# Kernel optimization log

Hardware: AMD Instinct MI355X
Metric: run time of the kernel (lower is better)

Reference implementation:

```python
import jax, jax.numpy as jnp
import numpy as np

B, N = 64, 128          # batch, nodes
D = 3                   # feature_dim
E = 1                   # edge_dim
M = 16                  # m_dim (lucidrains EGNN default)
L = 2                   # number_of_layers
EIN = 2 * D + 1 + E     # edge MLP input dim = 8


def setup_inputs() -> dict:
    key = jax.random.key(0)
    ks = jax.random.split(key, 24)
    s = 0.1

    def w(k, shape):
        return jax.random.normal(k, shape, dtype=jnp.float32) * s

    return {
        "t": jax.random.uniform(ks[0], (B, N, 1), dtype=jnp.float32),
        "coors": jax.random.normal(ks[1], (B, N, 2), dtype=jnp.float32),
        "vel": jax.random.normal(ks[2], (B, N, 2), dtype=jnp.float32),
        # per-layer EGNN params, stacked over L layers
        "We1": w(ks[3], (L, EIN, 2 * EIN)), "be1": jnp.zeros((L, 2 * EIN), jnp.float32),
        "We2": w(ks[4], (L, 2 * EIN, M)),   "be2": jnp.zeros((L, M), jnp.float32),
        "Wc1": w(ks[5], (L, M, 4 * M)),     "bc1": jnp.zeros((L, 4 * M), jnp.float32),
        "Wc2": w(ks[6], (L, 4 * M, 1)),     "bc2": jnp.zeros((L, 1), jnp.float32),
        "Wv": w(ks[7], (L, D, 1)),          "bv": jnp.ones((L, 1), jnp.float32),
        # 1x1 conv head (kernel size 1 -> plain channel matmul)
        "Wconv1": w(ks[8], (32, 4)), "bconv1": jnp.zeros((32,), jnp.float32),
        "Wconv2": w(ks[9], (4, 32)), "bconv2": jnp.zeros((4,), jnp.float32),
    }


def _egnn_forward(t, coors, vel, We1, be1, We2, be2, Wc1, bc1, Wc2, bc2, Wv, bv,
                  Wconv1, bconv1, Wconv2, bconv2):
    silu = jax.nn.silu
    selu = jax.nn.selu
    b, n, _ = coors.shape
    feats = jnp.broadcast_to(t, (b, n, D))          # t.repeat(1,1,feature_dim)
    edges = jnp.ones((b, n, n, E), dtype=coors.dtype)
    hi = jnp.broadcast_to(feats[:, :, None, :], (b, n, n, D))
    hj = jnp.broadcast_to(feats[:, None, :, :], (b, n, n, D))

    for l in range(L):
        rel = coors[:, :, None, :] - coors[:, None, :, :]      # b i j 2
        dist = jnp.sum(rel * rel, axis=-1, keepdims=True)      # b i j 1
        e_in = jnp.concatenate([hi, hj, dist, edges], axis=-1) # b i j 8
        # edge MLP: Linear -> SiLU -> Linear -> SiLU
        m = silu(e_in @ We1[l] + be1[l])
        m = silu(m @ We2[l] + be2[l])                          # b i j M
        # coors MLP: SiLU -> Linear -> SiLU -> Linear -> scalar weight per edge
        h = silu(silu(m) @ Wc1[l] + bc1[l])
        w_ij = (h @ Wc2[l] + bc2[l])[..., 0]                   # b i j
        agg = jnp.einsum('bij,bijc->bic', w_ij, rel)           # b i 2
        # velocity update: phi_v(h_i) * v_i + aggregated relative-coor messages
        phi_v = feats @ Wv[l] + bv[l]                          # b n 1
        vel = phi_v * vel + agg
        coors = coors + vel
        # EGNN_layer wrapper applies SELU to coors and vel
        coors = selu(coors)
        vel = selu(vel)

    # conv head: concat channels (coors 2 + vel 2 = 4), two 1x1 convs
    x = selu(jnp.concatenate([coors, vel], axis=-1))           # b n 4
    x = selu(jnp.einsum('bnc,oc->bno', x, Wconv1) + bconv1)    # b n 32
    y = jnp.einsum('bnc,oc->bno', x, Wconv2) + bconv2          # b n 4
    return y[..., 0:2], y[..., 2:4]


def reference(t, coors, vel, We1, be1, We2, be2, Wc1, bc1, Wc2, bc2, Wv, bv,
              Wconv1, bconv1, Wconv2, bconv2):
    return _egnn_forward(t, coors, vel, We1, be1, We2, be2, Wc1, bc1, Wc2, bc2,
                         Wv, bv, Wconv1, bconv1, Wconv2, bconv2)
```

## Files before the change

kernel.cpp:

```cpp
#include <hip/hip_runtime.h>


#define NB 64
#define NN 128

typedef __attribute__((ext_vector_type(8))) short short8;
typedef __attribute__((ext_vector_type(4))) float floatx4;

__device__ __forceinline__ unsigned short f2bf(float x) {
    unsigned u = __float_as_uint(x);
    return (unsigned short)((u + 0x7FFFu + ((u >> 16) & 1u)) >> 16);
}
__device__ __forceinline__ float bf2f(unsigned short b) {
    return __uint_as_float(((unsigned)b) << 16);
}
__device__ __forceinline__ unsigned pack2(float x, float y) {
    return (unsigned)f2bf(x) | ((unsigned)f2bf(y) << 16);
}
__device__ __forceinline__ float silu_f(float x) {
    float e = __expf(-x);
    return x * __builtin_amdgcn_rcpf(1.0f + e);
}
__device__ __forceinline__ float selu_f(float x) {
    const float alpha = 1.6732632423543772f;
    const float scale = 1.0507009873554805f;
    float neg = alpha * (__expf(x) - 1.0f);
    return scale * (x > 0.0f ? x : neg);
}

template <bool DO_HEAD>
__global__ __launch_bounds__(256) void egnn_layer(
    const float* __restrict__ t,
    const float* __restrict__ coors_in,
    const float* __restrict__ vel_in,
    const float* __restrict__ We1, const float* __restrict__ be1,
    const float* __restrict__ We2, const float* __restrict__ be2,
    const float* __restrict__ Wc1, const float* __restrict__ bc1,
    const float* __restrict__ Wc2, const float* __restrict__ bc2,
    const float* __restrict__ Wv,  const float* __restrict__ bv,
    const float* __restrict__ Wconv1, const float* __restrict__ bconv1,
    const float* __restrict__ Wconv2, const float* __restrict__ bconv2,
    int layer,
    float* __restrict__ coors_out, float* __restrict__ vel_out,
    float* __restrict__ out)
{
    const int l   = threadIdx.x & 63;
    const int wv  = threadIdx.x >> 6;
    const int row = blockIdx.x * 4 + wv;
    const int b   = row >> 7;
    const int i   = row & 127;
    const int q   = l >> 4;
    const int em  = l & 15;

    const float* We1l = We1 + layer * 8 * 16;
    const float* be1l = be1 + layer * 16;
    const float* We2l = We2 + layer * 16 * 16;
    const float* be2l = be2 + layer * 16;
    const float* Wc1l = Wc1 + layer * 16 * 64;
    const float* bc1l = bc1 + layer * 64;
    const float* Wc2l = Wc2 + layer * 64;
    const float  wv_s = Wv[layer * 3 + 0] + Wv[layer * 3 + 1] + Wv[layer * 3 + 2];
    const float  bvl  = bv[layer];

    float Aw = We1l[0 * 16 + em] + We1l[1 * 16 + em] + We1l[2 * 16 + em];
    float Bw = We1l[3 * 16 + em] + We1l[4 * 16 + em] + We1l[5 * 16 + em];
    float Cw = We1l[6 * 16 + em];
    unsigned short Ah = f2bf(Aw), Al = f2bf(Aw - bf2f(Ah));
    unsigned short Bh = f2bf(Bw), Bl = f2bf(Bw - bf2f(Bh));
    unsigned short Ch = f2bf(Cw), Cl = f2bf(Cw - bf2f(Ch));
    short8 wA;
    {
        short h0 = (q == 0) ? (short)Ah : ((q == 1) ? (short)Al : (short)0);
        short h1 = (q == 0) ? (short)Bh : ((q == 1) ? (short)Bl : (short)0);
        short h2 = (q == 0) ? (short)Ch : ((q == 1) ? (short)Cl : (short)0);
        wA[0] = h0; wA[1] = h0; wA[2] = h1; wA[3] = h1;
        wA[4] = h2; wA[5] = h2; wA[6] = 0;  wA[7] = 0;
    }
    floatx4 biasA;
#pragma unroll
    for (int r = 0; r < 4; ++r)
        biasA[r] = We1l[7 * 16 + 4 * q + r] + be1l[4 * q + r];

    short8 wB;
#pragma unroll
    for (int j = 0; j < 8; ++j) {
        int k = q * 8 + j;
        float w = We2l[(k & 15) * 16 + em];
        unsigned short hv = f2bf(w);
        unsigned short lv = f2bf(w - bf2f(hv));
        wB[j] = (k < 16) ? (short)hv : (short)lv;
    }
    floatx4 biasB;
#pragma unroll
    for (int r = 0; r < 4; ++r) biasB[r] = be2l[4 * q + r];

    short8 wC[4];
    floatx4 biasC[4];
    float wc2v[16];
#pragma unroll
    for (int f = 0; f < 4; ++f) {
#pragma unroll
        for (int j = 0; j < 8; ++j) {
            int k = q * 8 + j;
            float w = Wc1l[(k & 15) * 64 + 16 * f + em];
            unsigned short hv = f2bf(w);
            unsigned short lv = f2bf(w - bf2f(hv));
            wC[f][j] = (k < 16) ? (short)hv : (short)lv;
        }
#pragma unroll
        for (int r = 0; r < 4; ++r) {
            biasC[f][r]    = bc1l[16 * f + 4 * q + r];
            wc2v[f * 4 + r] = Wc2l[16 * f + 4 * q + r];
        }
    }
    const float bc2q = (q == 0) ? bc2[layer] : 0.0f;

    const float ti = t[b * NN + i];
    unsigned short tih = f2bf(ti), til = f2bf(ti - bf2f(tih));
    const float2* cin = (const float2*)coors_in + b * NN;
    const float2 ci = cin[i];

    const int sA = em + ((q & 1) << 5);
    const int sB = sA + 16;

    float ax = 0.0f, ay = 0.0f;

#pragma unroll 2
    for (int tt = 0; tt < 8; ++tt) {
        const int j = tt * 16 + em;
        const float tj = t[b * NN + j];
        const float2 cj = cin[j];
        const float rx = ci.x - cj.x, ry = ci.y - cj.y;
        const float dist = rx * rx + ry * ry;
        unsigned short tjh = f2bf(tj),   tjl = f2bf(tj - bf2f(tjh));
        unsigned short dh  = f2bf(dist), dl  = f2bf(dist - bf2f(dh));

        short8 bA;
        const bool act = (q < 2);
        bA[0] = act ? (short)tih : (short)0;
        bA[1] = act ? (short)til : (short)0;
        bA[2] = act ? (short)tjh : (short)0;
        bA[3] = act ? (short)tjl : (short)0;
        bA[4] = act ? (short)dh  : (short)0;
        bA[5] = act ? (short)dl  : (short)0;
        bA[6] = 0; bA[7] = 0;

        floatx4 accA = __builtin_amdgcn_mfma_f32_16x16x32_bf16(wA, bA, biasA, 0, 0, 0);
        unsigned P0 = pack2(silu_f(accA[0]), silu_f(accA[1]));
        unsigned P1 = pack2(silu_f(accA[2]), silu_f(accA[3]));
        uint4 tb;
        tb.x = (unsigned)__shfl((int)P0, sA, 64);
        tb.y = (unsigned)__shfl((int)P1, sA, 64);
        tb.z = (unsigned)__shfl((int)P0, sB, 64);
        tb.w = (unsigned)__shfl((int)P1, sB, 64);
        short8 bB = __builtin_bit_cast(short8, tb);

        floatx4 accB = __builtin_amdgcn_mfma_f32_16x16x32_bf16(wB, bB, biasB, 0, 0, 0);
        unsigned Q0 = pack2(silu_f(silu_f(accB[0])), silu_f(silu_f(accB[1])));
        unsigned Q1 = pack2(silu_f(silu_f(accB[2])), silu_f(silu_f(accB[3])));
        uint4 tc;
        tc.x = (unsigned)__shfl((int)Q0, sA, 64);
        tc.y = (unsigned)__shfl((int)Q1, sA, 64);
        tc.z = (unsigned)__shfl((int)Q0, sB, 64);
        tc.w = (unsigned)__shfl((int)Q1, sB, 64);
        short8 bC = __builtin_bit_cast(short8, tc);

        floatx4 h0 = __builtin_amdgcn_mfma_f32_16x16x32_bf16(wC[0], bC, biasC[0], 0, 0, 0);
        floatx4 h1 = __builtin_amdgcn_mfma_f32_16x16x32_bf16(wC[1], bC, biasC[1], 0, 0, 0);
        floatx4 h2 = __builtin_amdgcn_mfma_f32_16x16x32_bf16(wC[2], bC, biasC[2], 0, 0, 0);
        floatx4 h3 = __builtin_amdgcn_mfma_f32_16x16x32_bf16(wC[3], bC, biasC[3], 0, 0, 0);

        float wp = bc2q;
#pragma unroll
        for (int r = 0; r < 4; ++r) wp += silu_f(h0[r]) * wc2v[0 + r];
#pragma unroll
        for (int r = 0; r < 4; ++r) wp += silu_f(h1[r]) * wc2v[4 + r];
#pragma unroll
        for (int r = 0; r < 4; ++r) wp += silu_f(h2[r]) * wc2v[8 + r];
#pragma unroll
        for (int r = 0; r < 4; ++r) wp += silu_f(h3[r]) * wc2v[12 + r];

        ax += wp * rx;
        ay += wp * ry;
    }

#pragma unroll
    for (int m = 32; m >= 1; m >>= 1) {
        ax += __shfl_xor(ax, m, 64);
        ay += __shfl_xor(ay, m, 64);
    }

    if (l == 0) {
        const float2* vin = (const float2*)vel_in + b * NN;
        const float2 vi = vin[i];
        const float phi = ti * wv_s + bvl;
        float vx = phi * vi.x + ax;
        float vy = phi * vi.y + ay;
        float cx = ci.x + vx;
        float cy = ci.y + vy;
        cx = selu_f(cx); cy = selu_f(cy);
        vx = selu_f(vx); vy = selu_f(vy);
        if (!DO_HEAD) {
            float2* cout = (float2*)coors_out + b * NN;
            float2* vout = (float2*)vel_out + b * NN;
            cout[i] = make_float2(cx, cy);
            vout[i] = make_float2(vx, vy);
        } else {
            const float x0 = selu_f(cx), x1 = selu_f(cy);
            const float x2 = selu_f(vx), x3 = selu_f(vy);
            float y[4];
#pragma unroll
            for (int o = 0; o < 4; ++o) y[o] = bconv2[o];
#pragma unroll 8
            for (int c = 0; c < 32; ++c) {
                float xc = selu_f(bconv1[c] + x0 * Wconv1[c * 4 + 0]
                                            + x1 * Wconv1[c * 4 + 1]
                                            + x2 * Wconv1[c * 4 + 2]
                                            + x3 * Wconv1[c * 4 + 3]);
#pragma unroll
                for (int o = 0; o < 4; ++o) y[o] += xc * Wconv2[o * 32 + c];
            }
            const int idx = (b * NN + i) * 2;
            out[idx]     = y[0];
            out[idx + 1] = y[1];
            out[NB * NN * 2 + idx]     = y[2];
            out[NB * NN * 2 + idx + 1] = y[3];
        }
    }
}

extern "C" void kernel_launch(void* const* d_in, const int* in_sizes, int n_in,
                              void* d_out, int out_size, void* d_ws, size_t ws_size,
                              hipStream_t stream) {
    const float* t      = (const float*)d_in[0];
    const float* coors  = (const float*)d_in[1];
    const float* vel    = (const float*)d_in[2];
    const float* We1    = (const float*)d_in[3];
    const float* be1    = (const float*)d_in[4];
    const float* We2    = (const float*)d_in[5];
    const float* be2    = (const float*)d_in[6];
    const float* Wc1    = (const float*)d_in[7];
    const float* bc1    = (const float*)d_in[8];
    const float* Wc2    = (const float*)d_in[9];
    const float* bc2    = (const float*)d_in[10];
    const float* Wv     = (const float*)d_in[11];
    const float* bv     = (const float*)d_in[12];
    const float* Wconv1 = (const float*)d_in[13];
    const float* bconv1 = (const float*)d_in[14];
    const float* Wconv2 = (const float*)d_in[15];
    const float* bconv2 = (const float*)d_in[16];
    float* out = (float*)d_out;

    float* ws     = (float*)d_ws;
    float* coors1 = ws;
    float* vel1   = ws + NB * NN * 2;

    const dim3 grid(2048), block(256);

    egnn_layer<false><<<grid, block, 0, stream>>>(
        t, coors, vel, We1, be1, We2, be2, Wc1, bc1, Wc2, bc2, Wv, bv,
        Wconv1, bconv1, Wconv2, bconv2, 0, coors1, vel1, nullptr);

    egnn_layer<true><<<grid, block, 0, stream>>>(
        t, coors1, vel1, We1, be1, We2, be2, Wc1, bc1, Wc2, bc2, Wv, bv,
        Wconv1, bconv1, Wconv2, bconv2, 1, nullptr, nullptr, out);
}
```

Baseline: 177.5 us.

## Precompute split-bf16 weights in a prep kernel and replace first MFMA with FMAs

```diff
diff --git a/kernel.cpp b/kernel.cpp
--- a/kernel.cpp
+++ b/kernel.cpp
@@ -14,8 +14,10 @@
 __device__ __forceinline__ float bf2f(unsigned short b) {
     return __uint_as_float(((unsigned)b) << 16);
 }
-__device__ __forceinline__ unsigned pack2(float x, float y) {
-    return (unsigned)f2bf(x) | ((unsigned)f2bf(y) << 16);
+__device__ __forceinline__ unsigned packbf(float x, float y) {
+    unsigned xb = __float_as_uint(x) + 0x8000u;
+    unsigned yb = __float_as_uint(y) + 0x8000u;
+    return __builtin_amdgcn_perm(yb, xb, 0x07060302u);
 }
 __device__ __forceinline__ float silu_f(float x) {
     float e = __expf(-x);
@@ -28,14 +30,71 @@
     return scale * (x > 0.0f ? x : neg);
 }
 
+__global__ __launch_bounds__(128) void egnn_prep(
+    const float* __restrict__ We1, const float* __restrict__ be1,
+    const float* __restrict__ We2, const float* __restrict__ Wc1,
+    float* __restrict__ prep)
+{
+    const int layer = threadIdx.x >> 6;
+    const int l = threadIdx.x & 63;
+    const int q = l >> 4, em = l & 15;
+    const float* We1l = We1 + layer * 128;
+    const float* be1l = be1 + layer * 16;
+    const float* We2l = We2 + layer * 256;
+    const float* Wc1l = Wc1 + layer * 1024;
+    float* P = prep + layer * 2048;
+
+    if (l < 16) {
+        P[l]      = We1l[l] + We1l[16 + l] + We1l[32 + l];
+        P[16 + l] = We1l[48 + l] + We1l[64 + l] + We1l[80 + l];
+        P[32 + l] = We1l[96 + l];
+        P[48 + l] = We1l[112 + l] + be1l[l];
+    }
+    {
+        unsigned wb[4];
+#pragma unroll
+        for (int d = 0; d < 4; ++d) {
+            unsigned short sv[2];
+#pragma unroll
+            for (int e = 0; e < 2; ++e) {
+                int k = q * 8 + 2 * d + e;
+                float w = We2l[(k & 15) * 16 + em];
+                unsigned short hv = f2bf(w);
+                unsigned short lv = f2bf(w - bf2f(hv));
+                sv[e] = (k < 16) ? hv : lv;
+            }
+            wb[d] = (unsigned)sv[0] | ((unsigned)sv[1] << 16);
+        }
+        *(uint4*)((unsigned*)(P + 64) + l * 4) = make_uint4(wb[0], wb[1], wb[2], wb[3]);
+    }
+#pragma unroll
+    for (int f = 0; f < 4; ++f) {
+        unsigned wc[4];
+#pragma unroll
+        for (int d = 0; d < 4; ++d) {
+            unsigned short sv[2];
+#pragma unroll
+            for (int e = 0; e < 2; ++e) {
+                int k = q * 8 + 2 * d + e;
+                float w = Wc1l[(k & 15) * 64 + 16 * f + em];
+                unsigned short hv = f2bf(w);
+                unsigned short lv = f2bf(w - bf2f(hv));
+                sv[e] = (k < 16) ? hv : lv;
+            }
+            wc[d] = (unsigned)sv[0] | ((unsigned)sv[1] << 16);
+        }
+        *(uint4*)((unsigned*)(P + 320) + l * 16 + f * 4) = make_uint4(wc[0], wc[1], wc[2], wc[3]);
+    }
+}
+
 template <bool DO_HEAD>
 __global__ __launch_bounds__(256) void egnn_layer(
     const float* __restrict__ t,
     const float* __restrict__ coors_in,
     const float* __restrict__ vel_in,
-    const float* __restrict__ We1, const float* __restrict__ be1,
-    const float* __restrict__ We2, const float* __restrict__ be2,
-    const float* __restrict__ Wc1, const float* __restrict__ bc1,
+    const float* __restrict__ prep,
+    const float* __restrict__ be2,
+    const float* __restrict__ bc1,
     const float* __restrict__ Wc2, const float* __restrict__ bc2,
     const float* __restrict__ Wv,  const float* __restrict__ bv,
     const float* __restrict__ Wconv1, const float* __restrict__ bconv1,
@@ -45,78 +104,40 @@
     float* __restrict__ out)
 {
     const int l   = threadIdx.x & 63;
-    const int wv  = threadIdx.x >> 6;
-    const int row = blockIdx.x * 4 + wv;
+    const int wvi = threadIdx.x >> 6;
+    const int row = blockIdx.x * 4 + wvi;
     const int b   = row >> 7;
     const int i   = row & 127;
     const int q   = l >> 4;
     const int em  = l & 15;
 
-    const float* We1l = We1 + layer * 8 * 16;
-    const float* be1l = be1 + layer * 16;
-    const float* We2l = We2 + layer * 16 * 16;
+    const float* P    = prep + layer * 2048;
     const float* be2l = be2 + layer * 16;
-    const float* Wc1l = Wc1 + layer * 16 * 64;
     const float* bc1l = bc1 + layer * 64;
     const float* Wc2l = Wc2 + layer * 64;
     const float  wv_s = Wv[layer * 3 + 0] + Wv[layer * 3 + 1] + Wv[layer * 3 + 2];
     const float  bvl  = bv[layer];
 
-    float Aw = We1l[0 * 16 + em] + We1l[1 * 16 + em] + We1l[2 * 16 + em];
-    float Bw = We1l[3 * 16 + em] + We1l[4 * 16 + em] + We1l[5 * 16 + em];
-    float Cw = We1l[6 * 16 + em];
-    unsigned short Ah = f2bf(Aw), Al = f2bf(Aw - bf2f(Ah));
-    unsigned short Bh = f2bf(Bw), Bl = f2bf(Bw - bf2f(Bh));
-    unsigned short Ch = f2bf(Cw), Cl = f2bf(Cw - bf2f(Ch));
-    short8 wA;
-    {
-        short h0 = (q == 0) ? (short)Ah : ((q == 1) ? (short)Al : (short)0);
-        short h1 = (q == 0) ? (short)Bh : ((q == 1) ? (short)Bl : (short)0);
-        short h2 = (q == 0) ? (short)Ch : ((q == 1) ? (short)Cl : (short)0);
-        wA[0] = h0; wA[1] = h0; wA[2] = h1; wA[3] = h1;
-        wA[4] = h2; wA[5] = h2; wA[6] = 0;  wA[7] = 0;
-    }
-    floatx4 biasA;
-#pragma unroll
-    for (int r = 0; r < 4; ++r)
-        biasA[r] = We1l[7 * 16 + 4 * q + r] + be1l[4 * q + r];
-
-    short8 wB;
-#pragma unroll
-    for (int j = 0; j < 8; ++j) {
-        int k = q * 8 + j;
-        float w = We2l[(k & 15) * 16 + em];
-        unsigned short hv = f2bf(w);
-        unsigned short lv = f2bf(w - bf2f(hv));
-        wB[j] = (k < 16) ? (short)hv : (short)lv;
-    }
-    floatx4 biasB;
-#pragma unroll
-    for (int r = 0; r < 4; ++r) biasB[r] = be2l[4 * q + r];
-
+    const float4 a4 = *(const float4*)(P + 0  + q * 4);
+    const float4 b4 = *(const float4*)(P + 16 + q * 4);
+    const float4 c4 = *(const float4*)(P + 32 + q * 4);
+    const float4 d4 = *(const float4*)(P + 48 + q * 4);
+    const short8 wB = __builtin_bit_cast(short8, *(const uint4*)((const unsigned*)(P + 64) + l * 4));
     short8 wC[4];
+#pragma unroll
+    for (int f = 0; f < 4; ++f)
+        wC[f] = __builtin_bit_cast(short8, *(const uint4*)((const unsigned*)(P + 320) + l * 16 + f * 4));
+    const floatx4 biasB = __builtin_bit_cast(floatx4, *(const float4*)(be2l + q * 4));
     floatx4 biasC[4];
-    float wc2v[16];
+    float4 w2[4];
 #pragma unroll
     for (int f = 0; f < 4; ++f) {
-#pragma unroll
-        for (int j = 0; j < 8; ++j) {
-            int k = q * 8 + j;
-            float w = Wc1l[(k & 15) * 64 + 16 * f + em];
-            unsigned short hv = f2bf(w);
-            unsigned short lv = f2bf(w - bf2f(hv));
-            wC[f][j] = (k < 16) ? (short)hv : (short)lv;
-        }
-#pragma unroll
-        for (int r = 0; r < 4; ++r) {
-            biasC[f][r]    = bc1l[16 * f + 4 * q + r];
-            wc2v[f * 4 + r] = Wc2l[16 * f + 4 * q + r];
-        }
+        biasC[f] = __builtin_bit_cast(floatx4, *(const float4*)(bc1l + f * 16 + q * 4));
+        w2[f]    = *(const float4*)(Wc2l + f * 16 + q * 4);
     }
     const float bc2q = (q == 0) ? bc2[layer] : 0.0f;
 
     const float ti = t[b * NN + i];
-    unsigned short tih = f2bf(ti), til = f2bf(ti - bf2f(tih));
     const float2* cin = (const float2*)coors_in + b * NN;
     const float2 ci = cin[i];
 
@@ -132,22 +153,13 @@
         const float2 cj = cin[j];
         const float rx = ci.x - cj.x, ry = ci.y - cj.y;
         const float dist = rx * rx + ry * ry;
-        unsigned short tjh = f2bf(tj),   tjl = f2bf(tj - bf2f(tjh));
-        unsigned short dh  = f2bf(dist), dl  = f2bf(dist - bf2f(dh));
-
-        short8 bA;
-        const bool act = (q < 2);
-        bA[0] = act ? (short)tih : (short)0;
-        bA[1] = act ? (short)til : (short)0;
-        bA[2] = act ? (short)tjh : (short)0;
-        bA[3] = act ? (short)tjl : (short)0;
-        bA[4] = act ? (short)dh  : (short)0;
-        bA[5] = act ? (short)dl  : (short)0;
-        bA[6] = 0; bA[7] = 0;
-
-        floatx4 accA = __builtin_amdgcn_mfma_f32_16x16x32_bf16(wA, bA, biasA, 0, 0, 0);
-        unsigned P0 = pack2(silu_f(accA[0]), silu_f(accA[1]));
-        unsigned P1 = pack2(silu_f(accA[2]), silu_f(accA[3]));
+
+        float sA0 = fmaf(ti, a4.x, fmaf(tj, b4.x, fmaf(dist, c4.x, d4.x)));
+        float sA1 = fmaf(ti, a4.y, fmaf(tj, b4.y, fmaf(dist, c4.y, d4.y)));
+        float sA2 = fmaf(ti, a4.z, fmaf(tj, b4.z, fmaf(dist, c4.z, d4.z)));
+        float sA3 = fmaf(ti, a4.w, fmaf(tj, b4.w, fmaf(dist, c4.w, d4.w)));
+        unsigned P0 = packbf(silu_f(sA0), silu_f(sA1));
+        unsigned P1 = packbf(silu_f(sA2), silu_f(sA3));
         uint4 tb;
         tb.x = (unsigned)__shfl((int)P0, sA, 64);
         tb.y = (unsigned)__shfl((int)P1, sA, 64);
@@ -156,8 +168,8 @@
         short8 bB = __builtin_bit_cast(short8, tb);
 
         floatx4 accB = __builtin_amdgcn_mfma_f32_16x16x32_bf16(wB, bB, biasB, 0, 0, 0);
-        unsigned Q0 = pack2(silu_f(silu_f(accB[0])), silu_f(silu_f(accB[1])));
-        unsigned Q1 = pack2(silu_f(silu_f(accB[2])), silu_f(silu_f(accB[3])));
+        unsigned Q0 = packbf(silu_f(silu_f(accB[0])), silu_f(silu_f(accB[1])));
+        unsigned Q1 = packbf(silu_f(silu_f(accB[2])), silu_f(silu_f(accB[3])));
         uint4 tc;
         tc.x = (unsigned)__shfl((int)Q0, sA, 64);
         tc.y = (unsigned)__shfl((int)Q1, sA, 64);
@@ -172,16 +184,16 @@
 
         float wp = bc2q;
 #pragma unroll
-        for (int r = 0; r < 4; ++r) wp += silu_f(h0[r]) * wc2v[0 + r];
-#pragma unroll
-        for (int r = 0; r < 4; ++r) wp += silu_f(h1[r]) * wc2v[4 + r];
-#pragma unroll
-        for (int r = 0; r < 4; ++r) wp += silu_f(h2[r]) * wc2v[8 + r];
-#pragma unroll
-        for (int r = 0; r < 4; ++r) wp += silu_f(h3[r]) * wc2v[12 + r];
-
-        ax += wp * rx;
-        ay += wp * ry;
+        for (int r = 0; r < 4; ++r) wp = fmaf(silu_f(h0[r]), w2[0].x * 0.0f + ((const float*)&w2[0])[r], wp);
+#pragma unroll
+        for (int r = 0; r < 4; ++r) wp = fmaf(silu_f(h1[r]), ((const float*)&w2[1])[r], wp);
+#pragma unroll
+        for (int r = 0; r < 4; ++r) wp = fmaf(silu_f(h2[r]), ((const float*)&w2[2])[r], wp);
+#pragma unroll
+        for (int r = 0; r < 4; ++r) wp = fmaf(silu_f(h3[r]), ((const float*)&w2[3])[r], wp);
+
+        ax = fmaf(wp, rx, ax);
+        ay = fmaf(wp, ry, ay);
     }
 
 #pragma unroll
@@ -190,41 +202,40 @@
         ay += __shfl_xor(ay, m, 64);
     }
 
-    if (l == 0) {
-        const float2* vin = (const float2*)vel_in + b * NN;
-        const float2 vi = vin[i];
-        const float phi = ti * wv_s + bvl;
-        float vx = phi * vi.x + ax;
-        float vy = phi * vi.y + ay;
-        float cx = ci.x + vx;
-        float cy = ci.y + vy;
-        cx = selu_f(cx); cy = selu_f(cy);
-        vx = selu_f(vx); vy = selu_f(vy);
-        if (!DO_HEAD) {
-            float2* cout = (float2*)coors_out + b * NN;
-            float2* vout = (float2*)vel_out + b * NN;
-            cout[i] = make_float2(cx, cy);
-            vout[i] = make_float2(vx, vy);
-        } else {
-            const float x0 = selu_f(cx), x1 = selu_f(cy);
-            const float x2 = selu_f(vx), x3 = selu_f(vy);
-            float y[4];
-#pragma unroll
-            for (int o = 0; o < 4; ++o) y[o] = bconv2[o];
-#pragma unroll 8
-            for (int c = 0; c < 32; ++c) {
-                float xc = selu_f(bconv1[c] + x0 * Wconv1[c * 4 + 0]
-                                            + x1 * Wconv1[c * 4 + 1]
-                                            + x2 * Wconv1[c * 4 + 2]
-                                            + x3 * Wconv1[c * 4 + 3]);
-#pragma unroll
-                for (int o = 0; o < 4; ++o) y[o] += xc * Wconv2[o * 32 + c];
-            }
+    const float2 vi = ((const float2*)vel_in + b * NN)[i];
+    const float phi = ti * wv_s + bvl;
+    float vx = fmaf(phi, vi.x, ax);
+    float vy = fmaf(phi, vi.y, ay);
+    float cx = selu_f(ci.x + vx);
+    float cy = selu_f(ci.y + vy);
+    vx = selu_f(vx); vy = selu_f(vy);
+
+    if (!DO_HEAD) {
+        if (l == 0) {
+            ((float2*)coors_out + b * NN)[i] = make_float2(cx, cy);
+            ((float2*)vel_out + b * NN)[i]   = make_float2(vx, vy);
+        }
+    } else {
+        const float x0 = selu_f(cx), x1 = selu_f(cy);
+        const float x2 = selu_f(vx), x3 = selu_f(vy);
+        const int c = l & 31;
+        const float4 w1 = *(const float4*)(Wconv1 + c * 4);
+        const float xc = selu_f(bconv1[c] + fmaf(x0, w1.x, fmaf(x1, w1.y, fmaf(x2, w1.z, x3 * w1.w))));
+        float y0 = xc * Wconv2[c];
+        float y1 = xc * Wconv2[32 + c];
+        float y2 = xc * Wconv2[64 + c];
+        float y3 = xc * Wconv2[96 + c];
+#pragma unroll
+        for (int m = 16; m >= 1; m >>= 1) {
+            y0 += __shfl_xor(y0, m, 64);
+            y1 += __shfl_xor(y1, m, 64);
+            y2 += __shfl_xor(y2, m, 64);
+            y3 += __shfl_xor(y3, m, 64);
+        }
+        if (l == 0) {
             const int idx = (b * NN + i) * 2;
-            out[idx]     = y[0];
-            out[idx + 1] = y[1];
-            out[NB * NN * 2 + idx]     = y[2];
-            out[NB * NN * 2 + idx + 1] = y[3];
+            *(float2*)(out + idx) = make_float2(y0 + bconv2[0], y1 + bconv2[1]);
+            *(float2*)(out + NB * NN * 2 + idx) = make_float2(y2 + bconv2[2], y3 + bconv2[3]);
         }
     }
 }
@@ -254,14 +265,17 @@
     float* ws     = (float*)d_ws;
     float* coors1 = ws;
     float* vel1   = ws + NB * NN * 2;
+    float* prep   = ws + 2 * NB * NN * 2;
+
+    egnn_prep<<<dim3(1), dim3(128), 0, stream>>>(We1, be1, We2, Wc1, prep);
 
     const dim3 grid(2048), block(256);
 
     egnn_layer<false><<<grid, block, 0, stream>>>(
-        t, coors, vel, We1, be1, We2, be2, Wc1, bc1, Wc2, bc2, Wv, bv,
+        t, coors, vel, prep, be2, bc1, Wc2, bc2, Wv, bv,
         Wconv1, bconv1, Wconv2, bconv2, 0, coors1, vel1, nullptr);
 
     egnn_layer<true><<<grid, block, 0, stream>>>(
-        t, coors1, vel1, We1, be1, We2, be2, Wc1, bc1, Wc2, bc2, Wv, bv,
+        t, coors1, vel1, prep, be2, bc1, Wc2, bc2, Wv, bv,
         Wconv1, bconv1, Wconv2, bconv2, 1, nullptr, nullptr, out);
 }
```

Measured after the change: 152.8 us. 13.9% less time.
